# Performance work log

Measured on AMD Instinct MI355X. Metric: run time of the kernel, lower is better.

Reference implementation:

```python
import jax, jax.numpy as jnp
import numpy as np

D_MODEL = 1024
N_HEADS = 16
D_HEAD = D_MODEL // N_HEADS
LUT_SIZE = 4096
TWO_PI = 2.0 * np.pi
SCALE = np.sqrt(2.0 * D_HEAD).astype(np.float32)

# Global sin/cos lookup table over [0, 2*pi), 4096 entries (mirrors get_global_lut(4096)).
_GRID = (TWO_PI * np.arange(LUT_SIZE) / LUT_SIZE).astype(np.float32)
_SIN_TABLE = jnp.asarray(np.sin(_GRID))
_COS_TABLE = jnp.asarray(np.cos(_GRID))


def _lut_sin_cos(theta):
    # quantize angle to nearest LUT bin (wrap mod 2*pi) and gather
    idx = jnp.mod(jnp.round(theta * (LUT_SIZE / TWO_PI)).astype(jnp.int32), LUT_SIZE)
    return _SIN_TABLE[idx], _COS_TABLE[idx]


def setup_inputs() -> dict:
    key = jax.random.key(0)
    ks = jax.random.split(key, 7)
    B, S = 2, 2048
    x = jax.random.normal(ks[0], (B, S, D_MODEL), dtype=jnp.float32)
    w_q = 0.02 * jax.random.normal(ks[1], (N_HEADS, D_HEAD), dtype=jnp.float32)
    b_q = jnp.zeros((N_HEADS, D_HEAD), dtype=jnp.float32)
    w_k = 0.02 * jax.random.normal(ks[2], (N_HEADS, D_HEAD), dtype=jnp.float32)
    b_k = jnp.zeros((N_HEADS, D_HEAD), dtype=jnp.float32)
    v_w = jax.random.normal(ks[3], (D_MODEL, D_MODEL), dtype=jnp.float32) / np.sqrt(D_MODEL)
    out_w = jax.random.normal(ks[4], (D_MODEL, D_MODEL), dtype=jnp.float32) / np.sqrt(D_MODEL)
    return {"x": x, "w_q": w_q, "b_q": b_q, "w_k": w_k, "b_k": b_k, "v_w": v_w, "out_w": out_w}


def reference(x, w_q, b_q, w_k, b_k, v_w, out_w):
    B, S, D = x.shape
    x_heads = x.reshape(B, S, N_HEADS, D_HEAD)

    theta_q = x_heads / (1.0 + jnp.abs(w_q)) + b_q          # (B,S,H,dh)
    sin_q, cos_q = _lut_sin_cos(theta_q)
    Q = jnp.concatenate([cos_q, sin_q], axis=-1)            # (B,S,H,2dh)

    theta_k = x_heads / (1.0 + jnp.abs(w_k)) + b_k
    sin_k, cos_k = _lut_sin_cos(theta_k)
    K = jnp.concatenate([cos_k, sin_k], axis=-1)            # (B,S,H,2dh)

    V = (x @ v_w.T).reshape(B, S, N_HEADS, D_HEAD)          # (B,S,H,dh)

    scores = jnp.einsum("bqhe,bkhe->bhqk", Q, K) / SCALE    # (B,H,S,S)
    causal = jnp.triu(jnp.ones((S, S), dtype=bool), k=1)
    scores = jnp.where(causal, -jnp.inf, scores)
    attn = jax.nn.softmax(scores, axis=-1)

    out = jnp.einsum("bhqk,bkhd->bqhd", attn, V).reshape(B, S, D)
    return out @ out_w.T
```

## Files before the change

### kernel.cpp

```cpp
#include <hip/hip_runtime.h>
#include <hip/hip_bf16.h>
#include <math.h>


typedef __attribute__((ext_vector_type(8))) __bf16 bf16x8;
typedef __attribute__((ext_vector_type(4))) __bf16 bf16x4;
typedef __attribute__((ext_vector_type(4))) float f32x4;
typedef unsigned short ushort_t;
typedef unsigned int uint_t;

#define LUTC 651.8986469044033f
#define ANG 0.0015339807878856412f
#define QSCL 0.12751743590489435f

__device__ __forceinline__ float fast_exp2(float x) {
#if __has_builtin(__builtin_amdgcn_exp2f)
  return __builtin_amdgcn_exp2f(x);
#else
  return exp2f(x);
#endif
}

__device__ __forceinline__ ushort_t f2bf(float f) {
  union { __bf16 b; ushort_t u; } cv;
  cv.b = (__bf16)f;
  return cv.u;
}

__device__ __forceinline__ void store8(ushort_t* p, const ushort_t v[8]) {
  uint4 u;
  u.x = (uint_t)v[0] | ((uint_t)v[1] << 16);
  u.y = (uint_t)v[2] | ((uint_t)v[3] << 16);
  u.z = (uint_t)v[4] | ((uint_t)v[5] << 16);
  u.w = (uint_t)v[6] | ((uint_t)v[7] << 16);
  *(uint4*)p = u;
}

__device__ __forceinline__ void gl_lds16(const void* g, void* l) {
  __builtin_amdgcn_global_load_lds(
      (__attribute__((address_space(1))) void*)(g),
      (__attribute__((address_space(3))) void*)(l),
      16, 0, 0);
}

__global__ __launch_bounds__(256) void prep_kernel(
    const float* __restrict__ x, const float* __restrict__ wq, const float* __restrict__ bq,
    const float* __restrict__ wk, const float* __restrict__ bk,
    ushort_t* __restrict__ Qs, ushort_t* __restrict__ Ks, ushort_t* __restrict__ xb)
{
  int t = blockIdx.x * 256 + threadIdx.x;
  int dm8 = t & 127;
  int g = t >> 7;
  int dm0 = dm8 * 8;
  int h = dm0 >> 6;

  float aq[8], cq[8], ak[8], ck[8];
#pragma unroll
  for (int j = 0; j < 8; ++j) {
    aq[j] = LUTC / (1.0f + fabsf(wq[dm0 + j]));
    cq[j] = LUTC * bq[dm0 + j];
    ak[j] = LUTC / (1.0f + fabsf(wk[dm0 + j]));
    ck[j] = LUTC * bk[dm0 + j];
  }
  for (int i = 0; i < 4; ++i) {
    int bs = g * 4 + i;
    int b = bs >> 11, s = bs & 2047;
    const float4* xp4 = (const float4*)(x + (size_t)bs * 1024 + dm0);
    float4 xa = xp4[0], xbv4 = xp4[1];
    float xv[8] = {xa.x, xa.y, xa.z, xa.w, xbv4.x, xbv4.y, xbv4.z, xbv4.w};
    ushort_t qc[8], qs[8], kc[8], ks[8], xo[8];
#pragma unroll
    for (int j = 0; j < 8; ++j) {
      int iq = ((int)rintf(fmaf(xv[j], aq[j], cq[j]))) & 4095;
      float sq, cqv;
      __sincosf((float)iq * ANG, &sq, &cqv);
      int ik = ((int)rintf(fmaf(xv[j], ak[j], ck[j]))) & 4095;
      float sk, ckv;
      __sincosf((float)ik * ANG, &sk, &ckv);
      qc[j] = f2bf(cqv * QSCL);
      qs[j] = f2bf(sq * QSCL);
      kc[j] = f2bf(ckv);
      ks[j] = f2bf(sk);
      xo[j] = f2bf(xv[j]);
    }
    size_t qb = ((size_t)(b * 16 + h) * 2048 + s) * 128 + (dm0 & 63);
    store8(Qs + qb, qc);        store8(Qs + qb + 64, qs);
    store8(Ks + qb, kc);        store8(Ks + qb + 64, ks);
    store8(xb + (size_t)bs * 1024 + dm0, xo);
  }
}

__global__ __launch_bounds__(256) void wconv_kernel(
    const float* __restrict__ vw, const float* __restrict__ ow,
    ushort_t* __restrict__ vwb, ushort_t* __restrict__ owb)
{
  int t = blockIdx.x * 256 + threadIdx.x;
  const float* src;
  ushort_t* dst;
  int i;
  if (t < 131072) { src = vw; dst = vwb; i = t; }
  else            { src = ow; dst = owb; i = t - 131072; }
  const float4* p4 = (const float4*)(src + (size_t)i * 8);
  float4 a = p4[0], b = p4[1];
  float v[8] = {a.x, a.y, a.z, a.w, b.x, b.y, b.z, b.w};
  ushort_t o[8];
#pragma unroll
  for (int j = 0; j < 8; ++j) o[j] = f2bf(v[j]);
  store8(dst + (size_t)i * 8, o);
}

template <int EPI>
__global__ __launch_bounds__(256) void gemm_nt(
    const ushort_t* __restrict__ A, const ushort_t* __restrict__ B,
    float* __restrict__ Cf, ushort_t* __restrict__ Cb, int M, int N, int K)
{
  __shared__ __align__(16) ushort_t As[2][64 * 64];
  __shared__ __align__(16) ushort_t Bs[2][128 * 64];
  const int l = threadIdx.x & 63;
  const int w = threadIdx.x >> 6;
  const int g = l >> 4, lo = l & 15;
  const int mt = blockIdx.x % (M >> 6);
  const int nt = blockIdx.x / (M >> 6);
  const int m0 = mt << 6, n0 = nt << 7;

  const f32x4 zero4 = {0.f, 0.f, 0.f, 0.f};
  f32x4 acc[4][2];
#pragma unroll
  for (int i = 0; i < 4; ++i)
#pragma unroll
    for (int j = 0; j < 2; ++j) acc[i][j] = zero4;

  const int nk = K >> 6;

#define GEMM_STAGE(buf, k0_)                                                    \
  {                                                                             \
    int k0__ = (k0_);                                                           \
    _Pragma("unroll")                                                           \
    for (int i = 0; i < 2; ++i) {                                               \
      int ci = (w * 2 + i) * 64 + l;                                            \
      int r = ci >> 3, c = (ci & 7) ^ (r & 7);                                  \
      gl_lds16(A + (size_t)(m0 + r) * K + k0__ + c * 8, &As[buf][(w * 2 + i) * 512]); \
    }                                                                           \
    _Pragma("unroll")                                                           \
    for (int i = 0; i < 4; ++i) {                                               \
      int ci = (w * 4 + i) * 64 + l;                                            \
      int r = ci >> 3, c = (ci & 7) ^ (r & 7);                                  \
      gl_lds16(B + (size_t)(n0 + r) * K + k0__ + c * 8, &Bs[buf][(w * 4 + i) * 512]); \
    }                                                                           \
  }

  GEMM_STAGE(0, 0);
  GEMM_STAGE(1, 64);
  asm volatile("s_waitcnt vmcnt(6)" ::: "memory");
  __builtin_amdgcn_s_barrier();
  __builtin_amdgcn_sched_barrier(0);

  for (int t = 0; t < nk; ++t) {
    int cb = t & 1;
#pragma unroll
    for (int kk = 0; kk < 2; ++kk) {
      bf16x8 af[4], bfr[2];
#pragma unroll
      for (int mi = 0; mi < 4; ++mi) {
        int r = mi * 16 + lo;
        int ch = (g + 4 * kk) ^ (r & 7);
        af[mi] = *(const bf16x8*)&As[cb][r * 64 + ch * 8];
      }
#pragma unroll
      for (int ni = 0; ni < 2; ++ni) {
        int r = w * 32 + ni * 16 + lo;
        int ch = (g + 4 * kk) ^ (r & 7);
        bfr[ni] = *(const bf16x8*)&Bs[cb][r * 64 + ch * 8];
      }
#pragma unroll
      for (int mi = 0; mi < 4; ++mi)
#pragma unroll
        for (int ni = 0; ni < 2; ++ni)
          acc[mi][ni] = __builtin_amdgcn_mfma_f32_16x16x32_bf16(af[mi], bfr[ni], acc[mi][ni], 0, 0, 0);
    }
    __builtin_amdgcn_sched_barrier(0);
    asm volatile("s_waitcnt lgkmcnt(0)" ::: "memory");
    __builtin_amdgcn_s_barrier();
    if (t + 2 < nk) {
      GEMM_STAGE(cb, (t + 2) * 64);
      asm volatile("s_waitcnt vmcnt(6)" ::: "memory");
    } else {
      asm volatile("s_waitcnt vmcnt(0)" ::: "memory");
    }
    __builtin_amdgcn_s_barrier();
    __builtin_amdgcn_sched_barrier(0);
  }
#undef GEMM_STAGE

#pragma unroll
  for (int mi = 0; mi < 4; ++mi)
#pragma unroll
    for (int ni = 0; ni < 2; ++ni)
#pragma unroll
      for (int reg = 0; reg < 4; ++reg) {
        int row = m0 + mi * 16 + g * 4 + reg;
        int col = n0 + w * 32 + ni * 16 + lo;
        float v = acc[mi][ni][reg];
        if (EPI == 0) {
          Cf[(size_t)row * N + col] = v;
        } else {
          size_t o = (size_t)(col >> 11) * (1024 * 2048) + (size_t)row * 2048 + (col & 2047);
          Cb[o] = f2bf(v);
        }
      }
}


template<bool MASKED>
__device__ __forceinline__ void attn_tile(
    const ushort_t* __restrict__ Kc, const ushort_t* __restrict__ Vc,
    const bf16x8 (&qf)[2][4], f32x4 (&accO)[2][4], f32x4 (&acc_l)[2],
    int kb, int qw, int lo, int g, const bf16x8& ones)
{
  const f32x4 zero4 = {0.f, 0.f, 0.f, 0.f};
  f32x4 sc[2][4];
#pragma unroll
  for (int qm = 0; qm < 2; ++qm)
#pragma unroll
    for (int ns = 0; ns < 4; ++ns) sc[qm][ns] = zero4;

#pragma unroll
  for (int e = 0; e < 4; ++e) {
#pragma unroll
    for (int ns = 0; ns < 4; ++ns) {
      int kr = ns * 16 + lo;
      int cc = (g + 4 * e) ^ (kr & 7);
      bf16x8 kf = *(const bf16x8*)&Kc[kr * 128 + cc * 8];
#pragma unroll
      for (int qm = 0; qm < 2; ++qm)
        sc[qm][ns] = __builtin_amdgcn_mfma_f32_16x16x32_bf16(kf, qf[qm][e], sc[qm][ns], 0, 0, 0);
    }
  }

  bf16x8 pa[2][2];
#pragma unroll
  for (int qm = 0; qm < 2; ++qm) {
#pragma unroll
    for (int ns = 0; ns < 4; ++ns) {
#pragma unroll
      for (int reg = 0; reg < 4; ++reg) {
        float sv = sc[qm][ns][reg];
        if (MASKED) {
          int ka = kb + ns * 16 + g * 4 + reg;
          int qa = qw + qm * 16 + lo;
          sv = (ka <= qa) ? sv : -__builtin_inff();
        }
        pa[qm][ns >> 1][(ns & 1) * 4 + reg] = (__bf16)fast_exp2(sv);
      }
    }
  }

#pragma unroll
  for (int kk = 0; kk < 2; ++kk) {
#pragma unroll
    for (int nd = 0; nd < 4; ++nd) {
      int vr = nd * 16 + lo;
      int h8 = (g & 1) * 4;
      int cc0 = (4 * kk + (g >> 1)) ^ (vr & 7);
      int cc1 = (4 * kk + 2 + (g >> 1)) ^ (vr & 7);
      union { bf16x8 v8; bf16x4 v4[2]; } u;
      u.v4[0] = *(const bf16x4*)&Vc[vr * 64 + cc0 * 8 + h8];
      u.v4[1] = *(const bf16x4*)&Vc[vr * 64 + cc1 * 8 + h8];
#pragma unroll
      for (int qm = 0; qm < 2; ++qm)
        accO[qm][nd] = __builtin_amdgcn_mfma_f32_16x16x32_bf16(pa[qm][kk], u.v8, accO[qm][nd], 0, 0, 0);
    }
#pragma unroll
    for (int qm = 0; qm < 2; ++qm)
      acc_l[qm] = __builtin_amdgcn_mfma_f32_16x16x32_bf16(pa[qm][kk], ones, acc_l[qm], 0, 0, 0);
  }
}

__global__ __launch_bounds__(256) void attn_kernel(
    const ushort_t* __restrict__ Qs, const ushort_t* __restrict__ Ks,
    const ushort_t* __restrict__ Vt, ushort_t* __restrict__ Ob)
{
  const int S = 2048;
  const int id = blockIdx.x;
  const int bh = id & 31;
  const int qt = (id < 256) ? (15 - (id >> 5)) : ((id - 256) >> 5);
  const int l = threadIdx.x & 63;
  const int w = threadIdx.x >> 6;
  const int g = l >> 4, lo = l & 15;

  __shared__ __align__(16) ushort_t Kl[2][64 * 128];
  __shared__ __align__(16) ushort_t Vl[2][64 * 64];

  const int q0b = qt * 128;
  const int qw = q0b + w * 32;
  const ushort_t* Kbase = Ks + (size_t)bh * S * 128;
  const ushort_t* Vbase = Vt + (size_t)bh * 64 * S;

  bf16x8 ones;
#pragma unroll
  for (int j = 0; j < 8; ++j) ones[j] = (__bf16)1.0f;

  bf16x8 qf[2][4];
#pragma unroll
  for (int qm = 0; qm < 2; ++qm) {
    const ushort_t* qp = Qs + ((size_t)bh * S + qw + qm * 16 + lo) * 128 + 8 * g;
#pragma unroll
    for (int e = 0; e < 4; ++e) qf[qm][e] = *(const bf16x8*)(qp + 32 * e);
  }

  const f32x4 zero4 = {0.f, 0.f, 0.f, 0.f};
  f32x4 accO[2][4];
  f32x4 acc_l[2];
#pragma unroll
  for (int qm = 0; qm < 2; ++qm) {
    acc_l[qm] = zero4;
#pragma unroll
    for (int nd = 0; nd < 4; ++nd) accO[qm][nd] = zero4;
  }

  const int nt = 2 * qt + 2;

#define ATTN_STAGE(buf, kb_)                                                    \
  {                                                                             \
    int kb__ = (kb_);                                                           \
    _Pragma("unroll")                                                           \
    for (int i = 0; i < 4; ++i) {                                               \
      int ci = (w * 4 + i) * 64 + l;                                            \
      int r = ci >> 4, c = (ci & 15) ^ (r & 7);                                 \
      gl_lds16(Kbase + (size_t)(kb__ + r) * 128 + c * 8, &Kl[buf][(w * 4 + i) * 512]); \
    }                                                                           \
    _Pragma("unroll")                                                           \
    for (int i = 0; i < 2; ++i) {                                               \
      int ci = (w * 2 + i) * 64 + l;                                            \
      int r = ci >> 3, c = (ci & 7) ^ (r & 7);                                  \
      gl_lds16(Vbase + (size_t)r * S + kb__ + c * 8, &Vl[buf][(w * 2 + i) * 512]); \
    }                                                                           \
  }

  ATTN_STAGE(0, 0);
  ATTN_STAGE(1, 64);
  asm volatile("s_waitcnt vmcnt(6)" ::: "memory");
  __builtin_amdgcn_s_barrier();
  __builtin_amdgcn_sched_barrier(0);

  for (int t = 0; t < nt; ++t) {
    int cb = t & 1;
    __builtin_amdgcn_s_setprio(1);
    if (t < 2 * qt)
      attn_tile<false>(Kl[cb], Vl[cb], qf, accO, acc_l, t * 64, qw, lo, g, ones);
    else
      attn_tile<true>(Kl[cb], Vl[cb], qf, accO, acc_l, t * 64, qw, lo, g, ones);
    __builtin_amdgcn_s_setprio(0);
    __builtin_amdgcn_sched_barrier(0);
    asm volatile("s_waitcnt lgkmcnt(0)" ::: "memory");
    __builtin_amdgcn_s_barrier();
    if (t + 2 < nt) {
      ATTN_STAGE(cb, (t + 2) * 64);
      asm volatile("s_waitcnt vmcnt(6)" ::: "memory");
    } else {
      asm volatile("s_waitcnt vmcnt(0)" ::: "memory");
    }
    __builtin_amdgcn_s_barrier();
    __builtin_amdgcn_sched_barrier(0);
  }
#undef ATTN_STAGE

  float linv[2][4];
#pragma unroll
  for (int qm = 0; qm < 2; ++qm)
#pragma unroll
    for (int reg = 0; reg < 4; ++reg)
      linv[qm][reg] = 1.0f / acc_l[qm][reg];

  const int b = bh >> 4, h = bh & 15;
#pragma unroll
  for (int qm = 0; qm < 2; ++qm)
#pragma unroll
    for (int nd = 0; nd < 4; ++nd)
#pragma unroll
      for (int reg = 0; reg < 4; ++reg) {
        int q = qw + qm * 16 + g * 4 + reg;
        int d = nd * 16 + lo;
        Ob[((size_t)(b * 2048 + q)) * 1024 + h * 64 + d] = f2bf(accO[qm][nd][reg] * linv[qm][reg]);
      }
}

extern "C" void kernel_launch(void* const* d_in, const int* in_sizes, int n_in,
                              void* d_out, int out_size, void* d_ws, size_t ws_size,
                              hipStream_t stream) {
  const float* x  = (const float*)d_in[0];
  const float* wq = (const float*)d_in[1];
  const float* bq = (const float*)d_in[2];
  const float* wk = (const float*)d_in[3];
  const float* bk = (const float*)d_in[4];
  const float* vw = (const float*)d_in[5];
  const float* ow = (const float*)d_in[6];
  float* out = (float*)d_out;

  char* ws = (char*)d_ws;
  ushort_t* Qs  = (ushort_t*)(ws);
  ushort_t* Ksb = (ushort_t*)(ws + (16u << 20));
  ushort_t* Vtb = (ushort_t*)(ws + (32u << 20));
  ushort_t* xbb = (ushort_t*)(ws + (40u << 20));
  ushort_t* Obb = (ushort_t*)(ws + (48u << 20));
  ushort_t* vwb = (ushort_t*)(ws + (56u << 20));
  ushort_t* owb = (ushort_t*)(ws + (58u << 20));

  prep_kernel<<<512, 256, 0, stream>>>(x, wq, bq, wk, bk, Qs, Ksb, xbb);
  wconv_kernel<<<1024, 256, 0, stream>>>(vw, ow, vwb, owb);
  gemm_nt<1><<<512, 256, 0, stream>>>(vwb, xbb, nullptr, Vtb, 1024, 4096, 1024);
  attn_kernel<<<512, 256, 0, stream>>>(Qs, Ksb, Vtb, Obb);
  gemm_nt<0><<<512, 256, 0, stream>>>(Obb, owb, out, nullptr, 4096, 1024, 1024);
}
```

Measured before the change: 101.3 us.

## Split long causal attention rows into two KV halves and combine

The upper eight query tiles, which have the longest causal KV ranges, are now each split into two blocks that handle disjoint KV halves. One half writes unnormalized output to Ob and the other to a bf16 scratch buffer, each with its row sums, giving 768 blocks instead of 512 with shorter critical paths. A new combine kernel adds the two partial outputs and normalizes them. The kernel does not use a running max, so the partial sums add directly. The cost is an extra launch, extra memory traffic for the partials, and an extra bf16 rounding of the unnormalized partial outputs.

```diff
diff --git a/kernel.cpp b/kernel.cpp
--- a/kernel.cpp
+++ b/kernel.cpp
@@ -25,6 +25,12 @@
   union { __bf16 b; ushort_t u; } cv;
   cv.b = (__bf16)f;
   return cv.u;
+}
+
+__device__ __forceinline__ float bf2f(ushort_t u) {
+  union { float f; uint_t u; } cv;
+  cv.u = ((uint_t)u) << 16;
+  return cv.f;
 }
 
 __device__ __forceinline__ void store8(ushort_t* p, const ushort_t v[8]) {
@@ -278,12 +284,19 @@
 
 __global__ __launch_bounds__(256) void attn_kernel(
     const ushort_t* __restrict__ Qs, const ushort_t* __restrict__ Ks,
-    const ushort_t* __restrict__ Vt, ushort_t* __restrict__ Ob)
+    const ushort_t* __restrict__ Vt, ushort_t* __restrict__ Ob,
+    ushort_t* __restrict__ pnB, float* __restrict__ plA, float* __restrict__ plB)
 {
   const int S = 2048;
   const int id = blockIdx.x;
   const int bh = id & 31;
-  const int qt = (id < 256) ? (15 - (id >> 5)) : ((id - 256) >> 5);
+  const int seg = id >> 5;
+  int qt, k0, ntl, mode;
+  if (seg < 8)       { qt = 7 - seg;  k0 = 0;      ntl = 2 * qt + 2; mode = 0; }
+  else if (seg < 16) { qt = seg;      k0 = 0;      ntl = qt + 1;     mode = 1; }
+  else               { qt = seg - 8;  k0 = qt + 1; ntl = qt + 1;     mode = 2; }
+  const int p = bh * 8 + (qt - 8);
+
   const int l = threadIdx.x & 63;
   const int w = threadIdx.x >> 6;
   const int g = l >> 4, lo = l & 15;
@@ -291,8 +304,7 @@
   __shared__ __align__(16) ushort_t Kl[2][64 * 128];
   __shared__ __align__(16) ushort_t Vl[2][64 * 64];
 
-  const int q0b = qt * 128;
-  const int qw = q0b + w * 32;
+  const int qw = qt * 128 + w * 32;
   const ushort_t* Kbase = Ks + (size_t)bh * S * 128;
   const ushort_t* Vbase = Vt + (size_t)bh * 64 * S;
 
@@ -317,8 +329,6 @@
 #pragma unroll
     for (int nd = 0; nd < 4; ++nd) accO[qm][nd] = zero4;
   }
-
-  const int nt = 2 * qt + 2;
 
 #define ATTN_STAGE(buf, kb_)                                                    \
   {                                                                             \
@@ -337,25 +347,26 @@
     }                                                                           \
   }
 
-  ATTN_STAGE(0, 0);
-  ATTN_STAGE(1, 64);
+  ATTN_STAGE(0, k0 * 64);
+  ATTN_STAGE(1, (k0 + 1) * 64);
   asm volatile("s_waitcnt vmcnt(6)" ::: "memory");
   __builtin_amdgcn_s_barrier();
   __builtin_amdgcn_sched_barrier(0);
 
-  for (int t = 0; t < nt; ++t) {
+  for (int t = 0; t < ntl; ++t) {
     int cb = t & 1;
+    int gt = k0 + t;
     __builtin_amdgcn_s_setprio(1);
-    if (t < 2 * qt)
-      attn_tile<false>(Kl[cb], Vl[cb], qf, accO, acc_l, t * 64, qw, lo, g, ones);
+    if (gt < 2 * qt)
+      attn_tile<false>(Kl[cb], Vl[cb], qf, accO, acc_l, gt * 64, qw, lo, g, ones);
     else
-      attn_tile<true>(Kl[cb], Vl[cb], qf, accO, acc_l, t * 64, qw, lo, g, ones);
+      attn_tile<true>(Kl[cb], Vl[cb], qf, accO, acc_l, gt * 64, qw, lo, g, ones);
     __builtin_amdgcn_s_setprio(0);
     __builtin_amdgcn_sched_barrier(0);
     asm volatile("s_waitcnt lgkmcnt(0)" ::: "memory");
     __builtin_amdgcn_s_barrier();
-    if (t + 2 < nt) {
-      ATTN_STAGE(cb, (t + 2) * 64);
+    if (t + 2 < ntl) {
+      ATTN_STAGE(cb, (gt + 2) * 64);
       asm volatile("s_waitcnt vmcnt(6)" ::: "memory");
     } else {
       asm volatile("s_waitcnt vmcnt(0)" ::: "memory");
@@ -365,24 +376,93 @@
   }
 #undef ATTN_STAGE
 
-  float linv[2][4];
-#pragma unroll
-  for (int qm = 0; qm < 2; ++qm)
-#pragma unroll
-    for (int reg = 0; reg < 4; ++reg)
-      linv[qm][reg] = 1.0f / acc_l[qm][reg];
-
   const int b = bh >> 4, h = bh & 15;
-#pragma unroll
-  for (int qm = 0; qm < 2; ++qm)
-#pragma unroll
-    for (int nd = 0; nd < 4; ++nd)
-#pragma unroll
-      for (int reg = 0; reg < 4; ++reg) {
-        int q = qw + qm * 16 + g * 4 + reg;
-        int d = nd * 16 + lo;
-        Ob[((size_t)(b * 2048 + q)) * 1024 + h * 64 + d] = f2bf(accO[qm][nd][reg] * linv[qm][reg]);
-      }
+  if (mode == 0) {
+    float linv[2][4];
+#pragma unroll
+    for (int qm = 0; qm < 2; ++qm)
+#pragma unroll
+      for (int reg = 0; reg < 4; ++reg)
+        linv[qm][reg] = 1.0f / acc_l[qm][reg];
+#pragma unroll
+    for (int qm = 0; qm < 2; ++qm)
+#pragma unroll
+      for (int nd = 0; nd < 4; ++nd)
+#pragma unroll
+        for (int reg = 0; reg < 4; ++reg) {
+          int q = qw + qm * 16 + g * 4 + reg;
+          int d = nd * 16 + lo;
+          Ob[((size_t)(b * 2048 + q)) * 1024 + h * 64 + d] = f2bf(accO[qm][nd][reg] * linv[qm][reg]);
+        }
+  } else if (mode == 1) {
+#pragma unroll
+    for (int qm = 0; qm < 2; ++qm) {
+#pragma unroll
+      for (int nd = 0; nd < 4; ++nd)
+#pragma unroll
+        for (int reg = 0; reg < 4; ++reg) {
+          int q = qw + qm * 16 + g * 4 + reg;
+          int d = nd * 16 + lo;
+          Ob[((size_t)(b * 2048 + q)) * 1024 + h * 64 + d] = f2bf(accO[qm][nd][reg]);
+        }
+      if (lo == 0) {
+#pragma unroll
+        for (int reg = 0; reg < 4; ++reg)
+          plA[p * 128 + w * 32 + qm * 16 + g * 4 + reg] = acc_l[qm][reg];
+      }
+    }
+  } else {
+#pragma unroll
+    for (int qm = 0; qm < 2; ++qm) {
+#pragma unroll
+      for (int nd = 0; nd < 4; ++nd)
+#pragma unroll
+        for (int reg = 0; reg < 4; ++reg) {
+          int qr = w * 32 + qm * 16 + g * 4 + reg;
+          int d = nd * 16 + lo;
+          pnB[((size_t)p * 128 + qr) * 64 + d] = f2bf(accO[qm][nd][reg]);
+        }
+      if (lo == 0) {
+#pragma unroll
+        for (int reg = 0; reg < 4; ++reg)
+          plB[p * 128 + w * 32 + qm * 16 + g * 4 + reg] = acc_l[qm][reg];
+      }
+    }
+  }
+}
+
+__global__ __launch_bounds__(256) void combine_kernel(
+    ushort_t* __restrict__ Ob, const ushort_t* __restrict__ pnB,
+    const float* __restrict__ plA, const float* __restrict__ plB)
+{
+  int t = blockIdx.x * 256 + threadIdx.x;
+  int d0 = (t & 7) * 8;
+  int qidx = t >> 3;
+  int seg = qidx >> 7, qr = qidx & 127;
+  int bh = seg >> 3, j = seg & 7;
+  int qt = 8 + j;
+  int b = bh >> 4, h = bh & 15;
+  int qglob = qt * 128 + qr;
+
+  ushort_t* op = Ob + ((size_t)(b * 2048 + qglob)) * 1024 + h * 64 + d0;
+  const ushort_t* bp = pnB + ((size_t)seg * 128 + qr) * 64 + d0;
+  uint4 ua = *(const uint4*)op;
+  uint4 ub = *(const uint4*)bp;
+  float inv = 1.0f / (plA[seg * 128 + qr] + plB[seg * 128 + qr]);
+
+  const uint_t* pa = (const uint_t*)&ua;
+  const uint_t* pb = (const uint_t*)&ub;
+  ushort_t o[8];
+#pragma unroll
+  for (int i = 0; i < 4; ++i) {
+    float a0 = bf2f((ushort_t)(pa[i] & 0xffff));
+    float a1 = bf2f((ushort_t)(pa[i] >> 16));
+    float b0 = bf2f((ushort_t)(pb[i] & 0xffff));
+    float b1 = bf2f((ushort_t)(pb[i] >> 16));
+    o[2 * i]     = f2bf((a0 + b0) * inv);
+    o[2 * i + 1] = f2bf((a1 + b1) * inv);
+  }
+  store8(op, o);
 }
 
 extern "C" void kernel_launch(void* const* d_in, const int* in_sizes, int n_in,
@@ -406,9 +486,14 @@
   ushort_t* vwb = (ushort_t*)(ws + (56u << 20));
   ushort_t* owb = (ushort_t*)(ws + (58u << 20));
 
+  ushort_t* pnB = (ushort_t*)(ws + (40u << 20));
+  float*    plA = (float*)(ws + (40u << 20) + 4 * 1048576 + 262144);
+  float*    plB = (float*)(ws + (40u << 20) + 4 * 1048576 + 524288);
+
   prep_kernel<<<512, 256, 0, stream>>>(x, wq, bq, wk, bk, Qs, Ksb, xbb);
   wconv_kernel<<<1024, 256, 0, stream>>>(vw, ow, vwb, owb);
   gemm_nt<1><<<512, 256, 0, stream>>>(vwb, xbb, nullptr, Vtb, 1024, 4096, 1024);
-  attn_kernel<<<512, 256, 0, stream>>>(Qs, Ksb, Vtb, Obb);
+  attn_kernel<<<768, 256, 0, stream>>>(Qs, Ksb, Vtb, Obb, pnB, plA, plB);
+  combine_kernel<<<1024, 256, 0, stream>>>(Obb, pnB, plA, plB);
   gemm_nt<0><<<512, 256, 0, stream>>>(Obb, owb, out, nullptr, 4096, 1024, 1024);
 }
```

Measured after the change: 103.7 us. +2.4%, slower.
